# Optimization experiments

Hardware: AMD Instinct MI355X
Metric: run time of the kernel (lower is better)

The kernel has to match this reference:

```python
import jax, jax.numpy as jnp
import numpy as np

B, S, H = 1, 1024, 2048
NH, HD = 16, 128
E, K, FI, SFI = 8, 2, 1408, 2816
EPS = 1e-6
THETA = 10000.0


def setup_inputs() -> dict:
    key = jax.random.key(0)
    ks = jax.random.split(key, 14)
    sc = 0.02
    return {
        "hidden_states": jax.random.normal(ks[0], (B, S, H), jnp.float32),
        "ln1_w": jnp.ones((H,), jnp.float32),
        "ln2_w": jnp.ones((H,), jnp.float32),
        "wq": jax.random.normal(ks[1], (H, H), jnp.float32) * sc,
        "wk": jax.random.normal(ks[2], (H, H), jnp.float32) * sc,
        "wv": jax.random.normal(ks[3], (H, H), jnp.float32) * sc,
        "wo": jax.random.normal(ks[4], (H, H), jnp.float32) * sc,
        "gate_w": jax.random.normal(ks[5], (E, H), jnp.float32) * sc,
        "expert_gate": jax.random.normal(ks[6], (E, FI, H), jnp.float32) * sc,
        "expert_up": jax.random.normal(ks[7], (E, FI, H), jnp.float32) * sc,
        "expert_down": jax.random.normal(ks[8], (E, H, FI), jnp.float32) * sc,
        "shared_gate": jax.random.normal(ks[9], (SFI, H), jnp.float32) * sc,
        "shared_up": jax.random.normal(ks[10], (SFI, H), jnp.float32) * sc,
        "shared_down": jax.random.normal(ks[11], (H, SFI), jnp.float32) * sc,
    }


def _rmsnorm(x, w):
    v = jnp.mean(x * x, axis=-1, keepdims=True)
    return x * jax.lax.rsqrt(v + EPS) * w


def _rotate_half(x):
    x1, x2 = x[..., : HD // 2], x[..., HD // 2 :]
    return jnp.concatenate((-x2, x1), axis=-1)


def _rope_cos_sin():
    inv_freq = 1.0 / (THETA ** (jnp.arange(0, HD, 2, dtype=jnp.float32) / HD))
    t = jnp.arange(S, dtype=jnp.float32)
    freqs = t[:, None] * inv_freq[None, :]          # [S, HD//2]
    emb = jnp.concatenate((freqs, freqs), axis=-1)  # [S, HD]
    return jnp.cos(emb)[None, None], jnp.sin(emb)[None, None]  # [1,1,S,HD]


def _decoder_layer(hidden_states, ln1_w, ln2_w, wq, wk, wv, wo, gate_w,
                   expert_gate, expert_up, expert_down,
                   shared_gate, shared_up, shared_down):
    # ---- self-attention ----
    residual = hidden_states
    h = _rmsnorm(hidden_states, ln1_w)
    q = (h @ wq.T).reshape(B, S, NH, HD).transpose(0, 2, 1, 3)  # [B,NH,S,HD]
    k = (h @ wk.T).reshape(B, S, NH, HD).transpose(0, 2, 1, 3)
    v = (h @ wv.T).reshape(B, S, NH, HD).transpose(0, 2, 1, 3)
    cos, sin = _rope_cos_sin()
    q = q * cos + _rotate_half(q) * sin
    k = k * cos + _rotate_half(k) * sin
    scores = jnp.einsum('bhqd,bhkd->bhqk', q, k) / jnp.sqrt(jnp.float32(HD))
    causal = jnp.tril(jnp.ones((S, S), bool))
    scores = jnp.where(causal[None, None], scores, jnp.finfo(jnp.float32).min)
    probs = jax.nn.softmax(scores, axis=-1)
    attn = jnp.einsum('bhqk,bhkd->bhqd', probs, v)
    attn = attn.transpose(0, 2, 1, 3).reshape(B, S, H)
    x = residual + attn @ wo.T

    # ---- MoE MLP ----
    residual = x
    h2 = _rmsnorm(x, ln2_w)
    flat = h2.reshape(-1, H)                       # [N,H], N=B*S
    n_tok = flat.shape[0]
    logits = flat @ gate_w.T                       # [N,E]
    gate_scores = jax.nn.softmax(logits, axis=-1)
    topk_w, topk_idx = jax.lax.top_k(gate_scores, K)
    topk_w = topk_w / (jnp.sum(topk_w, axis=-1, keepdims=True) + 1e-20)
    # dense combine weights [N,E] (zero for unrouted experts)
    combine = jnp.zeros((n_tok, E), flat.dtype).at[
        jnp.arange(n_tok)[:, None], topk_idx].add(topk_w)
    # SwiGLU per expert, dense over all experts, then weighted combine
    g = jnp.einsum('nh,efh->enf', flat, expert_gate)   # [E,N,FI]
    u = jnp.einsum('nh,efh->enf', flat, expert_up)
    act = jax.nn.silu(g) * u
    eo = jnp.einsum('enf,ehf->enh', act, expert_down)  # [E,N,H]
    routed = jnp.einsum('enh,ne->nh', eo, combine)
    # shared experts (always on)
    shared = (jax.nn.silu(flat @ shared_gate.T) * (flat @ shared_up.T)) @ shared_down.T
    return residual + (routed + shared).reshape(B, S, H)


def reference(hidden_states, ln1_w, ln2_w, wq, wk, wv, wo, gate_w,
              expert_gate, expert_up, expert_down,
              shared_gate, shared_up, shared_down):
    return _decoder_layer(hidden_states, ln1_w, ln2_w, wq, wk, wv, wo, gate_w,
                          expert_gate, expert_up, expert_down,
                          shared_gate, shared_up, shared_down)
```

## Files before the change

### kernel.cpp

```cpp
#include <hip/hip_runtime.h>
#include <hip/hip_bf16.h>


#define DI __device__ __forceinline__

typedef __attribute__((ext_vector_type(8))) short short8;
typedef __attribute__((ext_vector_type(4))) float f32x4;
using u16 = unsigned short;

struct alignas(8) U16x4 { u16 x, y, z, w; };

DI u16 f2bf(float f) {
  unsigned u = __float_as_uint(f);
  u += 0x7fffu + ((u >> 16) & 1u);
  return (u16)(u >> 16);
}
DI float bf2f(u16 h) { return __uint_as_float(((unsigned)h) << 16); }
DI unsigned pack2(float f0, float f1) {
  unsigned a = __float_as_uint(f0) + 0x8000u;
  unsigned b = __float_as_uint(f1) + 0x8000u;
  return (a >> 16) | (b & 0xffff0000u);
}

DI void gload16(const void* g, void* l) {
  __builtin_amdgcn_global_load_lds((const __attribute__((address_space(1))) void*)g,
                                   (__attribute__((address_space(3))) void*)l, 16, 0, 0);
}


__global__ __launch_bounds__(256) void k_ropetab(float* __restrict__ tab) {
  int idx = blockIdx.x * 256 + threadIdx.x;
  int s = idx >> 6, i = idx & 63;
  double inv = pow(10000.0, -(double)(2 * i) / 128.0);
  double ang = (double)s * inv;
  tab[idx * 2 + 0] = (float)cos(ang);
  tab[idx * 2 + 1] = (float)sin(ang);
}

__global__ __launch_bounds__(256) void k_rmsnorm(const float* __restrict__ in,
                                                 const float* __restrict__ w,
                                                 float* __restrict__ outf,
                                                 u16* __restrict__ outh,
                                                 u16* __restrict__ outl) {
  const int row = blockIdx.x, t = threadIdx.x;
  const float* x = in + (size_t)row * 2048;
  float4 a = *(const float4*)&x[t * 4];
  float4 b = *(const float4*)&x[1024 + t * 4];
  float ss = a.x * a.x + a.y * a.y + a.z * a.z + a.w * a.w +
             b.x * b.x + b.y * b.y + b.z * b.z + b.w * b.w;
#pragma unroll
  for (int off = 32; off; off >>= 1) ss += __shfl_xor(ss, off);
  __shared__ float red[4];
  if ((t & 63) == 0) red[t >> 6] = ss;
  __syncthreads();
  float total = red[0] + red[1] + red[2] + red[3];
  float r = 1.0f / sqrtf(total * (1.0f / 2048.0f) + 1e-6f);
  float4 wa = *(const float4*)&w[t * 4];
  float4 wb = *(const float4*)&w[1024 + t * 4];
  float va[8] = {a.x * r * wa.x, a.y * r * wa.y, a.z * r * wa.z, a.w * r * wa.w,
                 b.x * r * wb.x, b.y * r * wb.y, b.z * r * wb.z, b.w * r * wb.w};
  if (outf) {
    *(float4*)&outf[(size_t)row * 2048 + t * 4] = make_float4(va[0], va[1], va[2], va[3]);
    *(float4*)&outf[(size_t)row * 2048 + 1024 + t * 4] = make_float4(va[4], va[5], va[6], va[7]);
  }
  if (outh) {
    U16x4 ha{f2bf(va[0]), f2bf(va[1]), f2bf(va[2]), f2bf(va[3])};
    U16x4 hb{f2bf(va[4]), f2bf(va[5]), f2bf(va[6]), f2bf(va[7])};
    *(U16x4*)&outh[(size_t)row * 2048 + t * 4] = ha;
    *(U16x4*)&outh[(size_t)row * 2048 + 1024 + t * 4] = hb;
    if (outl) {
      U16x4 la{f2bf(va[0] - bf2f(ha.x)), f2bf(va[1] - bf2f(ha.y)),
               f2bf(va[2] - bf2f(ha.z)), f2bf(va[3] - bf2f(ha.w))};
      U16x4 lb{f2bf(va[4] - bf2f(hb.x)), f2bf(va[5] - bf2f(hb.y)),
               f2bf(va[6] - bf2f(hb.z)), f2bf(va[7] - bf2f(hb.w))};
      *(U16x4*)&outl[(size_t)row * 2048 + t * 4] = la;
      *(U16x4*)&outl[(size_t)row * 2048 + 1024 + t * 4] = lb;
    }
  }
}

__global__ __launch_bounds__(256) void k_splitf4(
    const float* __restrict__ s0, const float* __restrict__ s1,
    const float* __restrict__ s2, const float* __restrict__ s3,
    u16* __restrict__ h0, u16* __restrict__ h1, u16* __restrict__ h2,
    u16* __restrict__ h3, u16* __restrict__ l0, u16* __restrict__ l1,
    u16* __restrict__ l2, u16* __restrict__ l3) {
  const int which = blockIdx.x >> 12;
  const int idx = ((blockIdx.x & 4095) * 256 + threadIdx.x) * 4;
  const float* src = (which == 0) ? s0 : (which == 1) ? s1 : (which == 2) ? s2 : s3;
  u16* dh = (which == 0) ? h0 : (which == 1) ? h1 : (which == 2) ? h2 : h3;
  u16* dl = (which == 0) ? l0 : (which == 1) ? l1 : (which == 2) ? l2 : l3;
  float4 v = *(const float4*)&src[idx];
  U16x4 h{f2bf(v.x), f2bf(v.y), f2bf(v.z), f2bf(v.w)};
  U16x4 l{f2bf(v.x - bf2f(h.x)), f2bf(v.y - bf2f(h.y)),
          f2bf(v.z - bf2f(h.z)), f2bf(v.w - bf2f(h.w))};
  *(U16x4*)&dh[idx] = h;
  *(U16x4*)&dl[idx] = l;
}

__global__ __launch_bounds__(256) void k_rope(float* __restrict__ q, float* __restrict__ k,
                                              const float* __restrict__ tab) {
  int idx = blockIdx.x * 256 + threadIdx.x;
  int s = idx >> 10, rem = idx & 1023;
  int h = rem >> 6, i = rem & 63;
  size_t base = (size_t)s * 2048 + h * 128 + i;
  float c = tab[(s * 64 + i) * 2 + 0];
  float sn = tab[(s * 64 + i) * 2 + 1];
  const float qs = 0.08838834764831845f;
  float q1 = q[base], q2 = q[base + 64];
  q[base] = (q1 * c - q2 * sn) * qs;
  q[base + 64] = (q2 * c + q1 * sn) * qs;
  float k1 = k[base], k2 = k[base + 64];
  k[base] = k1 * c - k2 * sn;
  k[base + 64] = k2 * c + k1 * sn;
}

__global__ __launch_bounds__(256) void k_splitkv(
    const float* __restrict__ qf, const float* __restrict__ kf,
    const float* __restrict__ vf,
    u16* __restrict__ Qh, u16* __restrict__ Ql,
    u16* __restrict__ Kh, u16* __restrict__ Kl,
    u16* __restrict__ Vth, u16* __restrict__ Vtl) {
  int idx = (blockIdx.x * 256 + threadIdx.x) * 4;
  int s = idx >> 11, c = idx & 2047;
  float4 q4 = *(const float4*)&qf[idx];
  U16x4 qh{f2bf(q4.x), f2bf(q4.y), f2bf(q4.z), f2bf(q4.w)};
  U16x4 ql{f2bf(q4.x - bf2f(qh.x)), f2bf(q4.y - bf2f(qh.y)),
           f2bf(q4.z - bf2f(qh.z)), f2bf(q4.w - bf2f(qh.w))};
  *(U16x4*)&Qh[idx] = qh; *(U16x4*)&Ql[idx] = ql;
  float4 k4 = *(const float4*)&kf[idx];
  U16x4 kh{f2bf(k4.x), f2bf(k4.y), f2bf(k4.z), f2bf(k4.w)};
  U16x4 kl{f2bf(k4.x - bf2f(kh.x)), f2bf(k4.y - bf2f(kh.y)),
           f2bf(k4.z - bf2f(kh.z)), f2bf(k4.w - bf2f(kh.w))};
  *(U16x4*)&Kh[idx] = kh; *(U16x4*)&Kl[idx] = kl;
  float4 v4 = *(const float4*)&vf[idx];
  float vv[4] = {v4.x, v4.y, v4.z, v4.w};
#pragma unroll
  for (int i = 0; i < 4; ++i) {
    u16 hv = f2bf(vv[i]);
    u16 lv = f2bf(vv[i] - bf2f(hv));
    Vth[(size_t)(c + i) * 1024 + s] = hv;
    Vtl[(size_t)(c + i) * 1024 + s] = lv;
  }
}

DI void stage_kv(const u16* __restrict__ Khg, const u16* __restrict__ Klg,
                 const u16* __restrict__ Vhg, const u16* __restrict__ Vlg,
                 u16* lsKh, u16* lsKl, u16* lsVh, u16* lsVl,
                 int kvb, int hh, int wv, int lane) {
#pragma unroll
  for (int it = 0; it < 4; ++it) {
    const int ebase = it * 2048 + wv * 512;
    const int eo = ebase + lane * 8;
    {
      const int rr = eo >> 7, cg = (eo >> 3) & 15;
      const size_t src = (size_t)(kvb + rr) * 2048 + hh * 128 + ((cg ^ (rr & 7)) << 3);
      gload16(Khg + src, lsKh + ebase);
      gload16(Klg + src, lsKl + ebase);
    }
    {
      const int rr = eo >> 6, cg = (eo >> 3) & 7;
      const size_t src = (size_t)(hh * 128 + rr) * 1024 + kvb + ((cg ^ (rr & 7)) << 3);
      gload16(Vhg + src, lsVh + ebase);
      gload16(Vlg + src, lsVl + ebase);
    }
  }
}

__global__ __launch_bounds__(256) void k_attn_tile(
    const u16* __restrict__ Qh, const u16* __restrict__ Ql,
    const u16* __restrict__ Khg, const u16* __restrict__ Klg,
    const u16* __restrict__ Vhg, const u16* __restrict__ Vlg,
    u16* __restrict__ atth, u16* __restrict__ attl) {
  __shared__ u16 lsKh[2][8192], lsKl[2][8192], lsVh[2][8192], lsVl[2][8192];
  __shared__ u16 Plh[4][16][72], Pll[4][16][72];
  const int hh = blockIdx.y;
  const int qb = blockIdx.x * 64;
  const int tid = threadIdx.x, lane = tid & 63, wv = tid >> 6;
  const int l15 = lane & 15, grp = lane >> 4;
  u16(*plh)[72] = Plh[wv];
  u16(*pll)[72] = Pll[wv];
  const int q_glob = qb + wv * 16 + l15;
  const int tend = blockIdx.x + 1;

  short8 qfh[4], qfl[4];
  const size_t qbase = (size_t)q_glob * 2048 + hh * 128;
#pragma unroll
  for (int c = 0; c < 4; ++c) {
    qfh[c] = *(const short8*)&Qh[qbase + c * 32 + grp * 8];
    qfl[c] = *(const short8*)&Ql[qbase + c * 32 + grp * 8];
  }
  f32x4 oacc[8];
#pragma unroll
  for (int dc = 0; dc < 8; ++dc) oacc[dc] = 0.f;
  float m_run = -1e30f, l_run = 0.f;

  int cur = 0;
  stage_kv(Khg, Klg, Vhg, Vlg, lsKh[0], lsKl[0], lsVh[0], lsVl[0], 0, hh, wv, lane);
  __syncthreads();

  for (int kt = 0; kt < tend; ++kt) {
    const int kvb = kt * 64;
    if (kt + 1 < tend)
      stage_kv(Khg, Klg, Vhg, Vlg, lsKh[cur ^ 1], lsKl[cur ^ 1], lsVh[cur ^ 1],
               lsVl[cur ^ 1], kvb + 64, hh, wv, lane);
    const u16* kh = lsKh[cur];
    const u16* kl = lsKl[cur];
    const u16* vh = lsVh[cur];
    const u16* vl = lsVl[cur];

    f32x4 s4[4];
#pragma unroll
    for (int sub = 0; sub < 4; ++sub) {
      f32x4 a = {0.f, 0.f, 0.f, 0.f};
      const int kr = sub * 16 + l15;
      const int sw = kr & 7;
#pragma unroll
      for (int c = 0; c < 4; ++c) {
        const int off = kr * 128 + ((((c << 2) | grp) ^ sw) << 3);
        short8 khf = *(const short8*)&kh[off];
        short8 klf = *(const short8*)&kl[off];
        a = __builtin_amdgcn_mfma_f32_16x16x32_bf16(khf, qfh[c], a, 0, 0, 0);
        a = __builtin_amdgcn_mfma_f32_16x16x32_bf16(klf, qfh[c], a, 0, 0, 0);
        a = __builtin_amdgcn_mfma_f32_16x16x32_bf16(khf, qfl[c], a, 0, 0, 0);
      }
      s4[sub] = a;
    }
    if (kt == tend - 1) {
#pragma unroll
      for (int sub = 0; sub < 4; ++sub)
#pragma unroll
        for (int r = 0; r < 4; ++r) {
          int kv = kvb + sub * 16 + grp * 4 + r;
          if (kv > q_glob) s4[sub][r] = -1e30f;
        }
    }
    float tmax = s4[0][0];
#pragma unroll
    for (int sub = 0; sub < 4; ++sub)
#pragma unroll
      for (int r = 0; r < 4; ++r) tmax = fmaxf(tmax, s4[sub][r]);
    tmax = fmaxf(tmax, __shfl_xor(tmax, 16));
    tmax = fmaxf(tmax, __shfl_xor(tmax, 32));
    float mnew = fmaxf(m_run, tmax);
    float scale = expf(m_run - mnew);
    float p[16], lsum = 0.f;
#pragma unroll
    for (int sub = 0; sub < 4; ++sub)
#pragma unroll
      for (int r = 0; r < 4; ++r) {
        float pe = expf(s4[sub][r] - mnew);
        p[sub * 4 + r] = pe;
        lsum += pe;
      }
    lsum += __shfl_xor(lsum, 16);
    lsum += __shfl_xor(lsum, 32);
    l_run = l_run * scale + lsum;
    m_run = mnew;
#pragma unroll
    for (int dc = 0; dc < 8; ++dc) oacc[dc] *= scale;
#pragma unroll
    for (int sub = 0; sub < 4; ++sub)
#pragma unroll
      for (int rp = 0; rp < 2; ++rp) {
        int i0 = sub * 4 + rp * 2;
        u16 h0 = f2bf(p[i0]), h1 = f2bf(p[i0 + 1]);
        u16 lo0 = f2bf(p[i0] - bf2f(h0)), lo1 = f2bf(p[i0 + 1] - bf2f(h1));
        int kvoff = sub * 16 + grp * 4 + rp * 2;
        *(unsigned*)&plh[l15][kvoff] = (unsigned)h0 | ((unsigned)h1 << 16);
        *(unsigned*)&pll[l15][kvoff] = (unsigned)lo0 | ((unsigned)lo1 << 16);
      }
    short8 phf[2], plf[2];
#pragma unroll
    for (int ks = 0; ks < 2; ++ks) {
      phf[ks] = *(const short8*)&plh[l15][ks * 32 + grp * 8];
      plf[ks] = *(const short8*)&pll[l15][ks * 32 + grp * 8];
    }
#pragma unroll
    for (int dc = 0; dc < 8; ++dc) {
      const int dr = dc * 16 + l15;
      const int sw = dr & 7;
      f32x4 acc = oacc[dc];
#pragma unroll
      for (int ks = 0; ks < 2; ++ks) {
        const int voff = dr * 64 + ((((ks << 2) | grp) ^ sw) << 3);
        short8 vhf = *(const short8*)&vh[voff];
        short8 vlf = *(const short8*)&vl[voff];
        acc = __builtin_amdgcn_mfma_f32_16x16x32_bf16(vhf, phf[ks], acc, 0, 0, 0);
        acc = __builtin_amdgcn_mfma_f32_16x16x32_bf16(vlf, phf[ks], acc, 0, 0, 0);
        acc = __builtin_amdgcn_mfma_f32_16x16x32_bf16(vhf, plf[ks], acc, 0, 0, 0);
      }
      oacc[dc] = acc;
    }
    __syncthreads();
    cur ^= 1;
  }
  float inv = 1.0f / l_run;
#pragma unroll
  for (int dc = 0; dc < 8; ++dc)
#pragma unroll
    for (int rp = 0; rp < 2; ++rp) {
      float v0 = oacc[dc][rp * 2] * inv;
      float v1 = oacc[dc][rp * 2 + 1] * inv;
      u16 h0 = f2bf(v0), h1 = f2bf(v1);
      u16 lo0 = f2bf(v0 - bf2f(h0)), lo1 = f2bf(v1 - bf2f(h1));
      size_t o = (size_t)q_glob * 2048 + hh * 128 + dc * 16 + grp * 4 + rp * 2;
      *(unsigned*)&atth[o] = (unsigned)h0 | ((unsigned)h1 << 16);
      *(unsigned*)&attl[o] = (unsigned)lo0 | ((unsigned)lo1 << 16);
    }
}

__global__ __launch_bounds__(256) void k_router(const float* __restrict__ h2f,
                                                const float* __restrict__ gw,
                                                int2* __restrict__ tidx,
                                                float2* __restrict__ twgt) {
  const int tok = blockIdx.x;
  const float* hrow = h2f + (size_t)tok * 2048;
  float part[8];
#pragma unroll
  for (int e = 0; e < 8; ++e) part[e] = 0.f;
  for (int j = 0; j < 8; ++j) {
    int p = j * 256 + threadIdx.x;
    float hv = hrow[p];
#pragma unroll
    for (int e = 0; e < 8; ++e) part[e] += hv * gw[e * 2048 + p];
  }
#pragma unroll
  for (int e = 0; e < 8; ++e)
#pragma unroll
    for (int off = 32; off; off >>= 1) part[e] += __shfl_xor(part[e], off);
  __shared__ float red[4][8];
  int wv = threadIdx.x >> 6, lane = threadIdx.x & 63;
  if (lane == 0) {
#pragma unroll
    for (int e = 0; e < 8; ++e) red[wv][e] = part[e];
  }
  __syncthreads();
  if (threadIdx.x == 0) {
    float lg[8];
#pragma unroll
    for (int e = 0; e < 8; ++e) lg[e] = red[0][e] + red[1][e] + red[2][e] + red[3][e];
    float m = lg[0];
#pragma unroll
    for (int e = 1; e < 8; ++e) m = fmaxf(m, lg[e]);
    float ex[8], s = 0.f;
#pragma unroll
    for (int e = 0; e < 8; ++e) { ex[e] = expf(lg[e] - m); s += ex[e]; }
#pragma unroll
    for (int e = 0; e < 8; ++e) ex[e] /= s;
    int i1 = 0;
#pragma unroll
    for (int e = 1; e < 8; ++e) if (ex[e] > ex[i1]) i1 = e;
    int i2 = (i1 == 0) ? 1 : 0;
#pragma unroll
    for (int e = 0; e < 8; ++e) if (e != i1 && ex[e] > ex[i2]) i2 = e;
    float s2 = ex[i1] + ex[i2] + 1e-20f;
    tidx[tok] = make_int2(i1, i2);
    twgt[tok] = make_float2(ex[i1] / s2, ex[i2] / s2);
  }
}

__global__ __launch_bounds__(64) void k_scan(const int2* __restrict__ tidx,
                                             const float2* __restrict__ twgt,
                                             int* __restrict__ meta,
                                             int* __restrict__ toklist,
                                             float* __restrict__ slotw,
                                             int* __restrict__ slots) {
  const int lane = threadIdx.x;
  int base = 0;
  for (int e = 0; e < 8; ++e) {
    int cnt = 0;
    for (int c = 0; c < 16; ++c) {
      const int tok = c * 64 + lane;
      int2 my = tidx[tok];
      int f1 = (my.x == e), f2 = (my.y == e);
      int flag = f1 | f2;
      unsigned long long m = __ballot(flag);
      if (flag) {
        float2 w = twgt[tok];
        int rank = (int)__popcll(m & ((1ull << lane) - 1ull));
        int s = base + cnt + rank;
        toklist[s] = tok;
        slotw[s] = f1 ? w.x : w.y;
        slots[tok * 2 + (f1 ? 0 : 1)] = s;
      }
      cnt += (int)__popcll(m);
    }
    if (lane == 0) { meta[e] = base; meta[9 + e] = cnt; }
    const int padded = ((cnt + 127) >> 7) << 7;
    for (int s = cnt + lane; s < padded; s += 64) {
      toklist[base + s] = 0;
      slotw[base + s] = 0.f;
    }
    base += padded;
  }
  if (lane == 0) meta[8] = base;
}


DI void stageA_bf16(const u16* __restrict__ A, size_t lda, int row0, int k0,
                    u16* lsA, int tid) {
  const int lane = tid & 63, wv = tid >> 6;
#pragma unroll
  for (int it = 0; it < 2; ++it) {
    const int ebase = it * 2048 + wv * 512;
    const int eo = ebase + lane * 8;
    const int rr = eo >> 5, cc = eo & 31;
    gload16(A + (size_t)(row0 + rr) * lda + k0 + cc, lsA + ebase);
  }
}

__global__ __launch_bounds__(256) void k_gemm_bf16split(
    const u16* __restrict__ Ah, const u16* __restrict__ Al,
    const u16* __restrict__ Bh0, const u16* __restrict__ Bl0,
    const u16* __restrict__ Bh1, const u16* __restrict__ Bl1,
    const u16* __restrict__ Bh2, const u16* __restrict__ Bl2,
    float* __restrict__ C0, float* __restrict__ C1, float* __restrict__ C2,
    const float* __restrict__ resid) {
  __shared__ u16 lsAh[4096], lsAl[4096], lsBh[4096], lsBl[4096];
  const int z = blockIdx.z;
  const u16* Bh = (z == 0) ? Bh0 : (z == 1) ? Bh1 : Bh2;
  const u16* Bl = (z == 0) ? Bl0 : (z == 1) ? Bl1 : Bl2;
  float* Cm = (z == 0) ? C0 : (z == 1) ? C1 : C2;
  const int tid = threadIdx.x, lane = tid & 63, wv = tid >> 6;
  const int wr = (wv >> 1) * 64, wc = (wv & 1) * 64;
  const int fr = lane & 15, fg = lane >> 4;
  const int row0 = blockIdx.x * 128, col0 = blockIdx.y * 128;
  f32x4 acc[4][4];
#pragma unroll
  for (int i = 0; i < 4; ++i)
#pragma unroll
    for (int j = 0; j < 4; ++j) acc[i][j] = 0.f;

  for (int kt = 0; kt < 64; ++kt) {
    const int k0 = kt * 32;
    stageA_bf16(Ah, 2048, row0, k0, lsAh, tid);
    stageA_bf16(Al, 2048, row0, k0, lsAl, tid);
    stageA_bf16(Bh, 2048, col0, k0, lsBh, tid);
    stageA_bf16(Bl, 2048, col0, k0, lsBl, tid);
    __syncthreads();
    short8 ah[4], al[4], bh[4], bl[4];
#pragma unroll
    for (int mi = 0; mi < 4; ++mi) {
      const int off = (wr + mi * 16 + fr) * 32 + fg * 8;
      ah[mi] = *(const short8*)&lsAh[off];
      al[mi] = *(const short8*)&lsAl[off];
    }
#pragma unroll
    for (int ni = 0; ni < 4; ++ni) {
      const int off = (wc + ni * 16 + fr) * 32 + fg * 8;
      bh[ni] = *(const short8*)&lsBh[off];
      bl[ni] = *(const short8*)&lsBl[off];
    }
#pragma unroll
    for (int mi = 0; mi < 4; ++mi)
#pragma unroll
      for (int ni = 0; ni < 4; ++ni) {
        f32x4 c = acc[mi][ni];
        c = __builtin_amdgcn_mfma_f32_16x16x32_bf16(al[mi], bh[ni], c, 0, 0, 0);
        c = __builtin_amdgcn_mfma_f32_16x16x32_bf16(ah[mi], bl[ni], c, 0, 0, 0);
        c = __builtin_amdgcn_mfma_f32_16x16x32_bf16(ah[mi], bh[ni], c, 0, 0, 0);
        acc[mi][ni] = c;
      }
    __syncthreads();
  }
  const bool hasres = (resid != nullptr);
#pragma unroll
  for (int mi = 0; mi < 4; ++mi)
#pragma unroll
    for (int ni = 0; ni < 4; ++ni)
#pragma unroll
      for (int qq = 0; qq < 4; ++qq) {
        const int row = row0 + wr + mi * 16 + fg * 4 + qq;
        const int col = col0 + wc + ni * 16 + fr;
        float val = acc[mi][ni][qq];
        if (hasres) val += resid[(size_t)row * 2048 + col];
        Cm[(size_t)row * 2048 + col] = val;
      }
}

DI int tile_to_expert(const int* meta, int t) {
  int e = 0;
  while (e < 7 && t >= (meta[e + 1] >> 7)) ++e;
  return e;
}

__global__ __launch_bounds__(256) void k_dual_all(
    const u16* __restrict__ h2b, const float* __restrict__ eg,
    const float* __restrict__ eu, const float* __restrict__ sg,
    const float* __restrict__ su, const int* __restrict__ meta,
    const int* __restrict__ toklist, const float* __restrict__ slotw,
    u16* __restrict__ act, u16* __restrict__ acts) {
  const int wid = blockIdx.x;
  const bool isShared = wid >= 528;
  __shared__ int toks[128];
  __shared__ u16 lsA[2][4096], lsG[2][2048], lsU[2][2048];
  const int tid = threadIdx.x, lane = tid & 63, wv = tid >> 6;
  const int wr = (wv >> 1) * 64, wc = (wv & 1) * 32;
  const int fr = lane & 15, fg = lane >> 4;

  int n0, off_e = 0, cnt_e = 0, rtile = 0;
  const float *Bg, *Bu;
  if (isShared) {
    const int b2 = wid - 528;
    rtile = b2 / 44;
    n0 = (b2 % 44) * 64;
    Bg = sg;
    Bu = su;
    if (tid < 128) toks[tid] = rtile * 128 + tid;
  } else {
    const int t = wid / 22;
    if (t >= (meta[8] >> 7)) return;
    n0 = (wid % 22) * 64;
    const int e = tile_to_expert(meta, t);
    off_e = meta[e];
    cnt_e = meta[9 + e];
    rtile = t - (off_e >> 7);
    Bg = eg + (size_t)e * 1408 * 2048;
    Bu = eu + (size_t)e * 1408 * 2048;
    if (tid < 128) toks[tid] = toklist[off_e + rtile * 128 + tid] & 1023;
  }
  f32x4 ag[4][2], au[4][2];
#pragma unroll
  for (int i = 0; i < 4; ++i)
#pragma unroll
    for (int j = 0; j < 2; ++j) { ag[i][j] = 0.f; au[i][j] = 0.f; }
  __syncthreads();

  const int ebase0 = wv * 512, ebase1 = 2048 + wv * 512;
  const int eoA0 = ebase0 + lane * 8, eoA1 = ebase1 + lane * 8;
  const u16* aS0 = h2b + (size_t)toks[eoA0 >> 5] * 2048 + (eoA0 & 31);
  const u16* aS1 = h2b + (size_t)toks[eoA1 >> 5] * 2048 + (eoA1 & 31);
  const int eoB0 = tid * 4, eoB1 = (256 + tid) * 4;
  const float* gB0 = Bg + (size_t)(n0 + (eoB0 >> 5)) * 2048 + (eoB0 & 31);
  const float* gB1 = Bg + (size_t)(n0 + (eoB1 >> 5)) * 2048 + (eoB1 & 31);
  const float* uB0 = Bu + (size_t)(n0 + (eoB0 >> 5)) * 2048 + (eoB0 & 31);
  const float* uB1 = Bu + (size_t)(n0 + (eoB1 >> 5)) * 2048 + (eoB1 & 31);

  float4 g0, g1, u0, u1;
  gload16(aS0, lsA[0] + ebase0);
  gload16(aS1, lsA[0] + ebase1);
  g0 = *(const float4*)gB0; g1 = *(const float4*)gB1;
  u0 = *(const float4*)uB0; u1 = *(const float4*)uB1;
  *(unsigned*)&lsG[0][eoB0] = pack2(g0.x, g0.y);
  *(unsigned*)&lsG[0][eoB0 + 2] = pack2(g0.z, g0.w);
  *(unsigned*)&lsG[0][eoB1] = pack2(g1.x, g1.y);
  *(unsigned*)&lsG[0][eoB1 + 2] = pack2(g1.z, g1.w);
  *(unsigned*)&lsU[0][eoB0] = pack2(u0.x, u0.y);
  *(unsigned*)&lsU[0][eoB0 + 2] = pack2(u0.z, u0.w);
  *(unsigned*)&lsU[0][eoB1] = pack2(u1.x, u1.y);
  *(unsigned*)&lsU[0][eoB1 + 2] = pack2(u1.z, u1.w);
  __syncthreads();

  int cur = 0;
  for (int kt = 0; kt < 64; ++kt) {
    const int k1 = (kt + 1) * 32;
    const bool pf = (kt + 1 < 64);
    if (pf) {
      gload16(aS0 + k1, lsA[cur ^ 1] + ebase0);
      gload16(aS1 + k1, lsA[cur ^ 1] + ebase1);
      g0 = *(const float4*)(gB0 + k1);
      g1 = *(const float4*)(gB1 + k1);
      u0 = *(const float4*)(uB0 + k1);
      u1 = *(const float4*)(uB1 + k1);
    }
    short8 af[4], gf[2], uf[2];
#pragma unroll
    for (int mi = 0; mi < 4; ++mi)
      af[mi] = *(const short8*)&lsA[cur][(wr + mi * 16 + fr) * 32 + fg * 8];
#pragma unroll
    for (int ni = 0; ni < 2; ++ni) {
      const int off = (wc + ni * 16 + fr) * 32 + fg * 8;
      gf[ni] = *(const short8*)&lsG[cur][off];
      uf[ni] = *(const short8*)&lsU[cur][off];
    }
#pragma unroll
    for (int mi = 0; mi < 4; ++mi)
#pragma unroll
      for (int ni = 0; ni < 2; ++ni) {
        ag[mi][ni] = __builtin_amdgcn_mfma_f32_16x16x32_bf16(af[mi], gf[ni], ag[mi][ni], 0, 0, 0);
        au[mi][ni] = __builtin_amdgcn_mfma_f32_16x16x32_bf16(af[mi], uf[ni], au[mi][ni], 0, 0, 0);
      }
    if (pf) {
      u16* lg = lsG[cur ^ 1];
      u16* lu = lsU[cur ^ 1];
      *(unsigned*)&lg[eoB0] = pack2(g0.x, g0.y);
      *(unsigned*)&lg[eoB0 + 2] = pack2(g0.z, g0.w);
      *(unsigned*)&lg[eoB1] = pack2(g1.x, g1.y);
      *(unsigned*)&lg[eoB1 + 2] = pack2(g1.z, g1.w);
      *(unsigned*)&lu[eoB0] = pack2(u0.x, u0.y);
      *(unsigned*)&lu[eoB0 + 2] = pack2(u0.z, u0.w);
      *(unsigned*)&lu[eoB1] = pack2(u1.x, u1.y);
      *(unsigned*)&lu[eoB1 + 2] = pack2(u1.z, u1.w);
    }
    __syncthreads();
    cur ^= 1;
  }
#pragma unroll
  for (int mi = 0; mi < 4; ++mi)
#pragma unroll
    for (int ni = 0; ni < 2; ++ni)
#pragma unroll
      for (int qq = 0; qq < 4; ++qq) {
        const int r = wr + mi * 16 + fg * 4 + qq;
        const int col = n0 + wc + ni * 16 + fr;
        float g = ag[mi][ni][qq], u = au[mi][ni][qq];
        float a = g / (1.0f + expf(-g)) * u;
        if (isShared) {
          acts[(size_t)(rtile * 128 + r) * 2816 + col] = f2bf(a);
        } else {
          const int rowInE = rtile * 128 + r;
          if (rowInE < cnt_e)
            act[(size_t)(off_e + rowInE) * 1408 + col] = f2bf(a * slotw[off_e + rowInE]);
        }
      }
}

__global__ __launch_bounds__(256) void k_down_all(
    const u16* __restrict__ act, const float* __restrict__ ed,
    const u16* __restrict__ acts, const float* __restrict__ sd,
    const int* __restrict__ meta, float* __restrict__ dwn,
    float* __restrict__ shd) {
  __shared__ u16 lsA[2][4096], lsB[2][4096];
  const int wid = blockIdx.x;
  const int tid = threadIdx.x, lane = tid & 63, wv = tid >> 6;
  const int fr = lane & 15, fg = lane >> 4;
  const int ebase0 = wv * 512, ebase1 = 2048 + wv * 512;
  const int eoA0 = ebase0 + lane * 8, eoA1 = ebase1 + lane * 8;
  if (wid < 384) {
    const int t = wid >> 4;
    if (t >= (meta[8] >> 7)) return;
    const int col0 = (wid & 15) * 128;
    const int e = tile_to_expert(meta, t);
    const int off_e = meta[e];
    const int rtile = t - (off_e >> 7);
    const int wr = (wv >> 1) * 64, wc = (wv & 1) * 64;
    const u16* Ab = act + (size_t)off_e * 1408;
    const float* Bb = ed + (size_t)e * 2048 * 1408;
    const u16* aS0 = Ab + (size_t)(rtile * 128 + (eoA0 >> 5)) * 1408 + (eoA0 & 31);
    const u16* aS1 = Ab + (size_t)(rtile * 128 + (eoA1 >> 5)) * 1408 + (eoA1 & 31);
    const float* bB[4];
    int eoB[4];
#pragma unroll
    for (int j = 0; j < 4; ++j) {
      eoB[j] = (j * 256 + tid) * 4;
      bB[j] = Bb + (size_t)(col0 + (eoB[j] >> 5)) * 1408 + (eoB[j] & 31);
    }
    f32x4 acc[4][4];
#pragma unroll
    for (int i = 0; i < 4; ++i)
#pragma unroll
      for (int j = 0; j < 4; ++j) acc[i][j] = 0.f;
    float4 bp[4];
    gload16(aS0, lsA[0] + ebase0);
    gload16(aS1, lsA[0] + ebase1);
#pragma unroll
    for (int j = 0; j < 4; ++j) bp[j] = *(const float4*)bB[j];
#pragma unroll
    for (int j = 0; j < 4; ++j) {
      *(unsigned*)&lsB[0][eoB[j]] = pack2(bp[j].x, bp[j].y);
      *(unsigned*)&lsB[0][eoB[j] + 2] = pack2(bp[j].z, bp[j].w);
    }
    __syncthreads();
    int cur = 0;
    for (int kt = 0; kt < 44; ++kt) {
      const int k1 = (kt + 1) * 32;
      const bool pf = (kt + 1 < 44);
      if (pf) {
        gload16(aS0 + k1, lsA[cur ^ 1] + ebase0);
        gload16(aS1 + k1, lsA[cur ^ 1] + ebase1);
#pragma unroll
        for (int j = 0; j < 4; ++j) bp[j] = *(const float4*)(bB[j] + k1);
      }
      short8 af[4], bf_[4];
#pragma unroll
      for (int mi = 0; mi < 4; ++mi)
        af[mi] = *(const short8*)&lsA[cur][(wr + mi * 16 + fr) * 32 + fg * 8];
#pragma unroll
      for (int ni = 0; ni < 4; ++ni)
        bf_[ni] = *(const short8*)&lsB[cur][(wc + ni * 16 + fr) * 32 + fg * 8];
#pragma unroll
      for (int mi = 0; mi < 4; ++mi)
#pragma unroll
        for (int ni = 0; ni < 4; ++ni)
          acc[mi][ni] = __builtin_amdgcn_mfma_f32_16x16x32_bf16(af[mi], bf_[ni], acc[mi][ni], 0, 0, 0);
      if (pf) {
        u16* lb = lsB[cur ^ 1];
#pragma unroll
        for (int j = 0; j < 4; ++j) {
          *(unsigned*)&lb[eoB[j]] = pack2(bp[j].x, bp[j].y);
          *(unsigned*)&lb[eoB[j] + 2] = pack2(bp[j].z, bp[j].w);
        }
      }
      __syncthreads();
      cur ^= 1;
    }
#pragma unroll
    for (int mi = 0; mi < 4; ++mi)
#pragma unroll
      for (int ni = 0; ni < 4; ++ni)
#pragma unroll
        for (int qq = 0; qq < 4; ++qq) {
          const int r = wr + mi * 16 + fg * 4 + qq;
          const int col = col0 + wc + ni * 16 + fr;
          dwn[(size_t)(off_e + rtile * 128 + r) * 2048 + col] = acc[mi][ni][qq];
        }
  } else {
    const int b2 = wid - 384;
    const int row0 = (b2 >> 5) * 128;
    const int col0 = (b2 & 31) * 64;
    const int wr = (wv >> 1) * 64, wc = (wv & 1) * 32;
    const u16* aS0 = acts + (size_t)(row0 + (eoA0 >> 5)) * 2816 + (eoA0 & 31);
    const u16* aS1 = acts + (size_t)(row0 + (eoA1 >> 5)) * 2816 + (eoA1 & 31);
    const float* bB[2];
    int eoB[2];
#pragma unroll
    for (int j = 0; j < 2; ++j) {
      eoB[j] = (j * 256 + tid) * 4;
      bB[j] = sd + (size_t)(col0 + (eoB[j] >> 5)) * 2816 + (eoB[j] & 31);
    }
    f32x4 acc[4][2];
#pragma unroll
    for (int i = 0; i < 4; ++i)
#pragma unroll
      for (int j = 0; j < 2; ++j) acc[i][j] = 0.f;
    float4 bp[2];
    gload16(aS0, lsA[0] + ebase0);
    gload16(aS1, lsA[0] + ebase1);
#pragma unroll
    for (int j = 0; j < 2; ++j) bp[j] = *(const float4*)bB[j];
#pragma unroll
    for (int j = 0; j < 2; ++j) {
      *(unsigned*)&lsB[0][eoB[j]] = pack2(bp[j].x, bp[j].y);
      *(unsigned*)&lsB[0][eoB[j] + 2] = pack2(bp[j].z, bp[j].w);
    }
    __syncthreads();
    int cur = 0;
    for (int kt = 0; kt < 88; ++kt) {
      const int k1 = (kt + 1) * 32;
      const bool pf = (kt + 1 < 88);
      if (pf) {
        gload16(aS0 + k1, lsA[cur ^ 1] + ebase0);
        gload16(aS1 + k1, lsA[cur ^ 1] + ebase1);
#pragma unroll
        for (int j = 0; j < 2; ++j) bp[j] = *(const float4*)(bB[j] + k1);
      }
      short8 af[4], bf_[2];
#pragma unroll
      for (int mi = 0; mi < 4; ++mi)
        af[mi] = *(const short8*)&lsA[cur][(wr + mi * 16 + fr) * 32 + fg * 8];
#pragma unroll
      for (int ni = 0; ni < 2; ++ni)
        bf_[ni] = *(const short8*)&lsB[cur][(wc + ni * 16 + fr) * 32 + fg * 8];
#pragma unroll
      for (int mi = 0; mi < 4; ++mi)
#pragma unroll
        for (int ni = 0; ni < 2; ++ni)
          acc[mi][ni] = __builtin_amdgcn_mfma_f32_16x16x32_bf16(af[mi], bf_[ni], acc[mi][ni], 0, 0, 0);
      if (pf) {
        u16* lb = lsB[cur ^ 1];
#pragma unroll
        for (int j = 0; j < 2; ++j) {
          *(unsigned*)&lb[eoB[j]] = pack2(bp[j].x, bp[j].y);
          *(unsigned*)&lb[eoB[j] + 2] = pack2(bp[j].z, bp[j].w);
        }
      }
      __syncthreads();
      cur ^= 1;
    }
#pragma unroll
    for (int mi = 0; mi < 4; ++mi)
#pragma unroll
      for (int ni = 0; ni < 2; ++ni)
#pragma unroll
        for (int qq = 0; qq < 4; ++qq) {
          const int row = row0 + wr + mi * 16 + fg * 4 + qq;
          const int col = col0 + wc + ni * 16 + fr;
          shd[(size_t)row * 2048 + col] = acc[mi][ni][qq];
        }
  }
}

__global__ __launch_bounds__(256) void k_combine(
    const float* __restrict__ shd, const float* __restrict__ x,
    const float* __restrict__ dwn, const int* __restrict__ slots,
    float* __restrict__ outp) {
  const int i4 = (blockIdx.x * 256 + threadIdx.x) * 4;
  const int row = i4 >> 11, col = i4 & 2047;
  const int s0 = slots[row * 2], s1 = slots[row * 2 + 1];
  float4 a = *(const float4*)&shd[i4];
  float4 b = *(const float4*)&x[i4];
  float4 c = *(const float4*)&dwn[(size_t)s0 * 2048 + col];
  float4 d = *(const float4*)&dwn[(size_t)s1 * 2048 + col];
  float4 o;
  o.x = a.x + b.x + c.x + d.x;
  o.y = a.y + b.y + c.y + d.y;
  o.z = a.z + b.z + c.z + d.z;
  o.w = a.w + b.w + c.w + d.w;
  *(float4*)&outp[i4] = o;
}


extern "C" void kernel_launch(void* const* d_in, const int* in_sizes, int n_in,
                              void* d_out, int out_size, void* d_ws, size_t ws_size,
                              hipStream_t stream) {
  (void)in_sizes; (void)n_in; (void)out_size; (void)ws_size;
  const float* hidden = (const float*)d_in[0];
  const float* ln1 = (const float*)d_in[1];
  const float* ln2 = (const float*)d_in[2];
  const float* wq = (const float*)d_in[3];
  const float* wk = (const float*)d_in[4];
  const float* wvw = (const float*)d_in[5];
  const float* wo = (const float*)d_in[6];
  const float* gw = (const float*)d_in[7];
  const float* eg = (const float*)d_in[8];
  const float* eu = (const float*)d_in[9];
  const float* ed = (const float*)d_in[10];
  const float* sg = (const float*)d_in[11];
  const float* su = (const float*)d_in[12];
  const float* sd = (const float*)d_in[13];
  float* out = (float*)d_out;
  char* ws = (char*)d_ws;

  const size_t KB = 1ull << 10, MB = 1ull << 20;
  float* tab = (float*)(ws + 0);
  int2* tidx = (int2*)(ws + 512 * KB);
  float2* twgt = (float2*)(ws + 520 * KB);
  int* meta = (int*)(ws + 528 * KB);
  int* tokl = (int*)(ws + 532 * KB);
  float* slw = (float*)(ws + 544 * KB);
  int* slots = (int*)(ws + 556 * KB);
  u16* hnh = (u16*)(ws + 1 * MB);
  u16* hnl = (u16*)(ws + 5 * MB);
  u16* wqh = (u16*)(ws + 9 * MB);
  u16* wql = (u16*)(ws + 17 * MB);
  u16* wkh = (u16*)(ws + 25 * MB);
  u16* wkl = (u16*)(ws + 33 * MB);
  u16* wvh = (u16*)(ws + 41 * MB);
  u16* wvl = (u16*)(ws + 49 * MB);
  u16* woh = (u16*)(ws + 57 * MB);
  u16* wol = (u16*)(ws + 65 * MB);
  float* qf = (float*)(ws + 73 * MB);
  float* kf = (float*)(ws + 81 * MB);
  float* vf = (float*)(ws + 89 * MB);
  u16* Qh = (u16*)(ws + 9 * MB);
  u16* Ql = (u16*)(ws + 13 * MB);
  u16* Kh = (u16*)(ws + 17 * MB);
  u16* Kl = (u16*)(ws + 21 * MB);
  u16* Vth = (u16*)(ws + 25 * MB);
  u16* Vtl = (u16*)(ws + 29 * MB);
  u16* atth = (u16*)(ws + 33 * MB);
  u16* attl = (u16*)(ws + 37 * MB);
  float* xf = (float*)(ws + 41 * MB);
  float* h2f = (float*)(ws + 49 * MB);
  u16* h2b = (u16*)(ws + 1 * MB);
  u16* act = (u16*)(ws + 73 * MB);
  u16* acts = (u16*)(ws + 82 * MB);
  float* dwn = (float*)(ws + 9 * MB);
  float* shd = (float*)(ws + 33 * MB);

  k_ropetab<<<256, 256, 0, stream>>>(tab);
  k_rmsnorm<<<1024, 256, 0, stream>>>(hidden, ln1, nullptr, hnh, hnl);
  k_splitf4<<<16384, 256, 0, stream>>>(wq, wk, wvw, wo, wqh, wkh, wvh, woh,
                                       wql, wkl, wvl, wol);
  k_gemm_bf16split<<<dim3(8, 16, 3), 256, 0, stream>>>(
      hnh, hnl, wqh, wql, wkh, wkl, wvh, wvl, qf, kf, vf, nullptr);
  k_rope<<<4096, 256, 0, stream>>>(qf, kf, tab);
  k_splitkv<<<2048, 256, 0, stream>>>(qf, kf, vf, Qh, Ql, Kh, Kl, Vth, Vtl);
  k_attn_tile<<<dim3(16, 16), 256, 0, stream>>>(Qh, Ql, Kh, Kl, Vth, Vtl, atth, attl);
  k_gemm_bf16split<<<dim3(8, 16, 1), 256, 0, stream>>>(
      atth, attl, woh, wol, woh, wol, woh, wol, xf, xf, xf, hidden);
  k_rmsnorm<<<1024, 256, 0, stream>>>(xf, ln2, h2f, h2b, nullptr);
  k_router<<<1024, 256, 0, stream>>>(h2f, gw, tidx, twgt);
  k_scan<<<1, 64, 0, stream>>>(tidx, twgt, meta, tokl, slw, slots);
  k_dual_all<<<880, 256, 0, stream>>>(h2b, eg, eu, sg, su, meta, tokl, slw, act, acts);
  k_down_all<<<640, 256, 0, stream>>>(act, ed, acts, sd, meta, dwn, shd);
  k_combine<<<2048, 256, 0, stream>>>(shd, xf, dwn, slots, out);
}
```

Measured before the change: 582.7 us.

## Halve split-bf16 GEMM column tile and drop double buffering in MoE kernels

The split-bf16 projection GEMMs now use 128x64 tiles instead of 128x128, doubling the grid so more workgroups are in flight. Separately, the expert dual (gate/up) and down kernels drop their LDS double buffering and register prefetch in favour of a simple load-sync-compute-sync loop. This lowers LDS use per block and may raise occupancy, but global loads are no longer overlapped with MFMA work and the smaller GEMM tile reloads the A panels more often.

After: 546.7 us. 6.2% less time.

```diff
diff --git a/kernel.cpp b/kernel.cpp
--- a/kernel.cpp
+++ b/kernel.cpp
@@ -417,29 +417,35 @@
     const u16* __restrict__ Bh2, const u16* __restrict__ Bl2,
     float* __restrict__ C0, float* __restrict__ C1, float* __restrict__ C2,
     const float* __restrict__ resid) {
-  __shared__ u16 lsAh[4096], lsAl[4096], lsBh[4096], lsBl[4096];
+  __shared__ u16 lsAh[4096], lsAl[4096], lsBh[2048], lsBl[2048];
   const int z = blockIdx.z;
   const u16* Bh = (z == 0) ? Bh0 : (z == 1) ? Bh1 : Bh2;
   const u16* Bl = (z == 0) ? Bl0 : (z == 1) ? Bl1 : Bl2;
   float* Cm = (z == 0) ? C0 : (z == 1) ? C1 : C2;
   const int tid = threadIdx.x, lane = tid & 63, wv = tid >> 6;
-  const int wr = (wv >> 1) * 64, wc = (wv & 1) * 64;
+  const int wr = (wv >> 1) * 64, wc = (wv & 1) * 32;
   const int fr = lane & 15, fg = lane >> 4;
-  const int row0 = blockIdx.x * 128, col0 = blockIdx.y * 128;
-  f32x4 acc[4][4];
+  const int row0 = blockIdx.x * 128, col0 = blockIdx.y * 64;
+  f32x4 acc[4][2];
 #pragma unroll
   for (int i = 0; i < 4; ++i)
 #pragma unroll
-    for (int j = 0; j < 4; ++j) acc[i][j] = 0.f;
+    for (int j = 0; j < 2; ++j) acc[i][j] = 0.f;
 
   for (int kt = 0; kt < 64; ++kt) {
     const int k0 = kt * 32;
     stageA_bf16(Ah, 2048, row0, k0, lsAh, tid);
     stageA_bf16(Al, 2048, row0, k0, lsAl, tid);
-    stageA_bf16(Bh, 2048, col0, k0, lsBh, tid);
-    stageA_bf16(Bl, 2048, col0, k0, lsBl, tid);
+    {
+      const int ebase = wv * 512;
+      const int eo = ebase + lane * 8;
+      const int rr = eo >> 5, cc = eo & 31;
+      const size_t src = (size_t)(col0 + rr) * 2048 + k0 + cc;
+      gload16(Bh + src, lsBh + ebase);
+      gload16(Bl + src, lsBl + ebase);
+    }
     __syncthreads();
-    short8 ah[4], al[4], bh[4], bl[4];
+    short8 ah[4], al[4], bh[2], bl[2];
 #pragma unroll
     for (int mi = 0; mi < 4; ++mi) {
       const int off = (wr + mi * 16 + fr) * 32 + fg * 8;
@@ -447,7 +453,7 @@
       al[mi] = *(const short8*)&lsAl[off];
     }
 #pragma unroll
-    for (int ni = 0; ni < 4; ++ni) {
+    for (int ni = 0; ni < 2; ++ni) {
       const int off = (wc + ni * 16 + fr) * 32 + fg * 8;
       bh[ni] = *(const short8*)&lsBh[off];
       bl[ni] = *(const short8*)&lsBl[off];
@@ -455,7 +461,7 @@
 #pragma unroll
     for (int mi = 0; mi < 4; ++mi)
 #pragma unroll
-      for (int ni = 0; ni < 4; ++ni) {
+      for (int ni = 0; ni < 2; ++ni) {
         f32x4 c = acc[mi][ni];
         c = __builtin_amdgcn_mfma_f32_16x16x32_bf16(al[mi], bh[ni], c, 0, 0, 0);
         c = __builtin_amdgcn_mfma_f32_16x16x32_bf16(ah[mi], bl[ni], c, 0, 0, 0);
@@ -468,7 +474,7 @@
 #pragma unroll
   for (int mi = 0; mi < 4; ++mi)
 #pragma unroll
-    for (int ni = 0; ni < 4; ++ni)
+    for (int ni = 0; ni < 2; ++ni)
 #pragma unroll
       for (int qq = 0; qq < 4; ++qq) {
         const int row = row0 + wr + mi * 16 + fg * 4 + qq;
@@ -494,7 +500,7 @@
   const int wid = blockIdx.x;
   const bool isShared = wid >= 528;
   __shared__ int toks[128];
-  __shared__ u16 lsA[2][4096], lsG[2][2048], lsU[2][2048];
+  __shared__ u16 lsA[4096], lsG[2048], lsU[2048];
   const int tid = threadIdx.x, lane = tid & 63, wv = tid >> 6;
   const int wr = (wv >> 1) * 64, wc = (wv & 1) * 32;
   const int fr = lane & 15, fg = lane >> 4;
@@ -537,42 +543,32 @@
   const float* uB0 = Bu + (size_t)(n0 + (eoB0 >> 5)) * 2048 + (eoB0 & 31);
   const float* uB1 = Bu + (size_t)(n0 + (eoB1 >> 5)) * 2048 + (eoB1 & 31);
 
-  float4 g0, g1, u0, u1;
-  gload16(aS0, lsA[0] + ebase0);
-  gload16(aS1, lsA[0] + ebase1);
-  g0 = *(const float4*)gB0; g1 = *(const float4*)gB1;
-  u0 = *(const float4*)uB0; u1 = *(const float4*)uB1;
-  *(unsigned*)&lsG[0][eoB0] = pack2(g0.x, g0.y);
-  *(unsigned*)&lsG[0][eoB0 + 2] = pack2(g0.z, g0.w);
-  *(unsigned*)&lsG[0][eoB1] = pack2(g1.x, g1.y);
-  *(unsigned*)&lsG[0][eoB1 + 2] = pack2(g1.z, g1.w);
-  *(unsigned*)&lsU[0][eoB0] = pack2(u0.x, u0.y);
-  *(unsigned*)&lsU[0][eoB0 + 2] = pack2(u0.z, u0.w);
-  *(unsigned*)&lsU[0][eoB1] = pack2(u1.x, u1.y);
-  *(unsigned*)&lsU[0][eoB1 + 2] = pack2(u1.z, u1.w);
-  __syncthreads();
-
-  int cur = 0;
   for (int kt = 0; kt < 64; ++kt) {
-    const int k1 = (kt + 1) * 32;
-    const bool pf = (kt + 1 < 64);
-    if (pf) {
-      gload16(aS0 + k1, lsA[cur ^ 1] + ebase0);
-      gload16(aS1 + k1, lsA[cur ^ 1] + ebase1);
-      g0 = *(const float4*)(gB0 + k1);
-      g1 = *(const float4*)(gB1 + k1);
-      u0 = *(const float4*)(uB0 + k1);
-      u1 = *(const float4*)(uB1 + k1);
-    }
+    const int k0 = kt * 32;
+    gload16(aS0 + k0, lsA + ebase0);
+    gload16(aS1 + k0, lsA + ebase1);
+    float4 g0 = *(const float4*)(gB0 + k0);
+    float4 g1 = *(const float4*)(gB1 + k0);
+    float4 u0 = *(const float4*)(uB0 + k0);
+    float4 u1 = *(const float4*)(uB1 + k0);
+    *(unsigned*)&lsG[eoB0] = pack2(g0.x, g0.y);
+    *(unsigned*)&lsG[eoB0 + 2] = pack2(g0.z, g0.w);
+    *(unsigned*)&lsG[eoB1] = pack2(g1.x, g1.y);
+    *(unsigned*)&lsG[eoB1 + 2] = pack2(g1.z, g1.w);
+    *(unsigned*)&lsU[eoB0] = pack2(u0.x, u0.y);
+    *(unsigned*)&lsU[eoB0 + 2] = pack2(u0.z, u0.w);
+    *(unsigned*)&lsU[eoB1] = pack2(u1.x, u1.y);
+    *(unsigned*)&lsU[eoB1 + 2] = pack2(u1.z, u1.w);
+    __syncthreads();
     short8 af[4], gf[2], uf[2];
 #pragma unroll
     for (int mi = 0; mi < 4; ++mi)
-      af[mi] = *(const short8*)&lsA[cur][(wr + mi * 16 + fr) * 32 + fg * 8];
+      af[mi] = *(const short8*)&lsA[(wr + mi * 16 + fr) * 32 + fg * 8];
 #pragma unroll
     for (int ni = 0; ni < 2; ++ni) {
       const int off = (wc + ni * 16 + fr) * 32 + fg * 8;
-      gf[ni] = *(const short8*)&lsG[cur][off];
-      uf[ni] = *(const short8*)&lsU[cur][off];
+      gf[ni] = *(const short8*)&lsG[off];
+      uf[ni] = *(const short8*)&lsU[off];
     }
 #pragma unroll
     for (int mi = 0; mi < 4; ++mi)
@@ -581,20 +577,7 @@
         ag[mi][ni] = __builtin_amdgcn_mfma_f32_16x16x32_bf16(af[mi], gf[ni], ag[mi][ni], 0, 0, 0);
         au[mi][ni] = __builtin_amdgcn_mfma_f32_16x16x32_bf16(af[mi], uf[ni], au[mi][ni], 0, 0, 0);
       }
-    if (pf) {
-      u16* lg = lsG[cur ^ 1];
-      u16* lu = lsU[cur ^ 1];
-      *(unsigned*)&lg[eoB0] = pack2(g0.x, g0.y);
-      *(unsigned*)&lg[eoB0 + 2] = pack2(g0.z, g0.w);
-      *(unsigned*)&lg[eoB1] = pack2(g1.x, g1.y);
-      *(unsigned*)&lg[eoB1 + 2] = pack2(g1.z, g1.w);
-      *(unsigned*)&lu[eoB0] = pack2(u0.x, u0.y);
-      *(unsigned*)&lu[eoB0 + 2] = pack2(u0.z, u0.w);
-      *(unsigned*)&lu[eoB1] = pack2(u1.x, u1.y);
-      *(unsigned*)&lu[eoB1 + 2] = pack2(u1.z, u1.w);
-    }
     __syncthreads();
-    cur ^= 1;
   }
 #pragma unroll
   for (int mi = 0; mi < 4; ++mi)
@@ -621,7 +604,7 @@
     const u16* __restrict__ acts, const float* __restrict__ sd,
     const int* __restrict__ meta, float* __restrict__ dwn,
     float* __restrict__ shd) {
-  __shared__ u16 lsA[2][4096], lsB[2][4096];
+  __shared__ u16 lsA[4096], lsB[4096];
   const int wid = blockIdx.x;
   const int tid = threadIdx.x, lane = tid & 63, wv = tid >> 6;
   const int fr = lane & 15, fg = lane >> 4;
@@ -651,49 +634,32 @@
     for (int i = 0; i < 4; ++i)
 #pragma unroll
       for (int j = 0; j < 4; ++j) acc[i][j] = 0.f;
-    float4 bp[4];
-    gload16(aS0, lsA[0] + ebase0);
-    gload16(aS1, lsA[0] + ebase1);
-#pragma unroll
-    for (int j = 0; j < 4; ++j) bp[j] = *(const float4*)bB[j];
-#pragma unroll
-    for (int j = 0; j < 4; ++j) {
-      *(unsigned*)&lsB[0][eoB[j]] = pack2(bp[j].x, bp[j].y);
-      *(unsigned*)&lsB[0][eoB[j] + 2] = pack2(bp[j].z, bp[j].w);
-    }
-    __syncthreads();
-    int cur = 0;
     for (int kt = 0; kt < 44; ++kt) {
-      const int k1 = (kt + 1) * 32;
-      const bool pf = (kt + 1 < 44);
-      if (pf) {
-        gload16(aS0 + k1, lsA[cur ^ 1] + ebase0);
-        gload16(aS1 + k1, lsA[cur ^ 1] + ebase1);
-#pragma unroll
-        for (int j = 0; j < 4; ++j) bp[j] = *(const float4*)(bB[j] + k1);
-      }
+      const int k0 = kt * 32;
+      gload16(aS0 + k0, lsA + ebase0);
+      gload16(aS1 + k0, lsA + ebase1);
+      float4 bp[4];
+#pragma unroll
+      for (int j = 0; j < 4; ++j) bp[j] = *(const float4*)(bB[j] + k0);
+#pragma unroll
+      for (int j = 0; j < 4; ++j) {
+        *(unsigned*)&lsB[eoB[j]] = pack2(bp[j].x, bp[j].y);
+        *(unsigned*)&lsB[eoB[j] + 2] = pack2(bp[j].z, bp[j].w);
+      }
+      __syncthreads();
       short8 af[4], bf_[4];
 #pragma unroll
       for (int mi = 0; mi < 4; ++mi)
-        af[mi] = *(const short8*)&lsA[cur][(wr + mi * 16 + fr) * 32 + fg * 8];
+        af[mi] = *(const short8*)&lsA[(wr + mi * 16 + fr) * 32 + fg * 8];
 #pragma unroll
       for (int ni = 0; ni < 4; ++ni)
-        bf_[ni] = *(const short8*)&lsB[cur][(wc + ni * 16 + fr) * 32 + fg * 8];
+        bf_[ni] = *(const short8*)&lsB[(wc + ni * 16 + fr) * 32 + fg * 8];
 #pragma unroll
       for (int mi = 0; mi < 4; ++mi)
 #pragma unroll
         for (int ni = 0; ni < 4; ++ni)
           acc[mi][ni] = __builtin_amdgcn_mfma_f32_16x16x32_bf16(af[mi], bf_[ni], acc[mi][ni], 0, 0, 0);
-      if (pf) {
-        u16* lb = lsB[cur ^ 1];
-#pragma unroll
-        for (int j = 0; j < 4; ++j) {
-          *(unsigned*)&lb[eoB[j]] = pack2(bp[j].x, bp[j].y);
-          *(unsigned*)&lb[eoB[j] + 2] = pack2(bp[j].z, bp[j].w);
-        }
-      }
       __syncthreads();
-      cur ^= 1;
     }
 #pragma unroll
     for (int mi = 0; mi < 4; ++mi)
@@ -724,49 +690,32 @@
     for (int i = 0; i < 4; ++i)
 #pragma unroll
       for (int j = 0; j < 2; ++j) acc[i][j] = 0.f;
-    float4 bp[2];
-    gload16(aS0, lsA[0] + ebase0);
-    gload16(aS1, lsA[0] + ebase1);
-#pragma unroll
-    for (int j = 0; j < 2; ++j) bp[j] = *(const float4*)bB[j];
-#pragma unroll
-    for (int j = 0; j < 2; ++j) {
-      *(unsigned*)&lsB[0][eoB[j]] = pack2(bp[j].x, bp[j].y);
-      *(unsigned*)&lsB[0][eoB[j] + 2] = pack2(bp[j].z, bp[j].w);
-    }
-    __syncthreads();
-    int cur = 0;
     for (int kt = 0; kt < 88; ++kt) {
-      const int k1 = (kt + 1) * 32;
-      const bool pf = (kt + 1 < 88);
-      if (pf) {
-        gload16(aS0 + k1, lsA[cur ^ 1] + ebase0);
-        gload16(aS1 + k1, lsA[cur ^ 1] + ebase1);
-#pragma unroll
-        for (int j = 0; j < 2; ++j) bp[j] = *(const float4*)(bB[j] + k1);
-      }
+      const int k0 = kt * 32;
+      gload16(aS0 + k0, lsA + ebase0);
+      gload16(aS1 + k0, lsA + ebase1);
+      float4 bp[2];
+#pragma unroll
+      for (int j = 0; j < 2; ++j) bp[j] = *(const float4*)(bB[j] + k0);
+#pragma unroll
+      for (int j = 0; j < 2; ++j) {
+        *(unsigned*)&lsB[eoB[j]] = pack2(bp[j].x, bp[j].y);
+        *(unsigned*)&lsB[eoB[j] + 2] = pack2(bp[j].z, bp[j].w);
+      }
+      __syncthreads();
       short8 af[4], bf_[2];
 #pragma unroll
       for (int mi = 0; mi < 4; ++mi)
-        af[mi] = *(const short8*)&lsA[cur][(wr + mi * 16 + fr) * 32 + fg * 8];
+        af[mi] = *(const short8*)&lsA[(wr + mi * 16 + fr) * 32 + fg * 8];
 #pragma unroll
       for (int ni = 0; ni < 2; ++ni)
-        bf_[ni] = *(const short8*)&lsB[cur][(wc + ni * 16 + fr) * 32 + fg * 8];
+        bf_[ni] = *(const short8*)&lsB[(wc + ni * 16 + fr) * 32 + fg * 8];
 #pragma unroll
       for (int mi = 0; mi < 4; ++mi)
 #pragma unroll
         for (int ni = 0; ni < 2; ++ni)
           acc[mi][ni] = __builtin_amdgcn_mfma_f32_16x16x32_bf16(af[mi], bf_[ni], acc[mi][ni], 0, 0, 0);
-      if (pf) {
-        u16* lb = lsB[cur ^ 1];
-#pragma unroll
-        for (int j = 0; j < 2; ++j) {
-          *(unsigned*)&lb[eoB[j]] = pack2(bp[j].x, bp[j].y);
-          *(unsigned*)&lb[eoB[j] + 2] = pack2(bp[j].z, bp[j].w);
-        }
-      }
       __syncthreads();
-      cur ^= 1;
     }
 #pragma unroll
     for (int mi = 0; mi < 4; ++mi)
@@ -863,12 +812,12 @@
   k_rmsnorm<<<1024, 256, 0, stream>>>(hidden, ln1, nullptr, hnh, hnl);
   k_splitf4<<<16384, 256, 0, stream>>>(wq, wk, wvw, wo, wqh, wkh, wvh, woh,
                                        wql, wkl, wvl, wol);
-  k_gemm_bf16split<<<dim3(8, 16, 3), 256, 0, stream>>>(
+  k_gemm_bf16split<<<dim3(8, 32, 3), 256, 0, stream>>>(
       hnh, hnl, wqh, wql, wkh, wkl, wvh, wvl, qf, kf, vf, nullptr);
   k_rope<<<4096, 256, 0, stream>>>(qf, kf, tab);
   k_splitkv<<<2048, 256, 0, stream>>>(qf, kf, vf, Qh, Ql, Kh, Kl, Vth, Vtl);
   k_attn_tile<<<dim3(16, 16), 256, 0, stream>>>(Qh, Ql, Kh, Kl, Vth, Vtl, atth, attl);
-  k_gemm_bf16split<<<dim3(8, 16, 1), 256, 0, stream>>>(
+  k_gemm_bf16split<<<dim3(8, 32, 1), 256, 0, stream>>>(
       atth, attl, woh, wol, woh, wol, woh, wol, xf, xf, xf, hidden);
   k_rmsnorm<<<1024, 256, 0, stream>>>(xf, ln2, h2f, h2b, nullptr);
   k_router<<<1024, 256, 0, stream>>>(h2f, gw, tidx, twgt);
```
